# Performance work log

Measured on AMD Instinct MI355X. Metric: run time of the kernel, lower is better.

Reference implementation:

```python
import jax, jax.numpy as jnp
import numpy as np

B, N, F_IN, D = 32, 100, 10, 64
TAU = 10.0
ALPHA = 0.2  # GAT leaky-relu slope
EPS = 1e-8


def _cosine_sim(e):
    n = e / (jnp.linalg.norm(e, axis=-1, keepdims=True) + EPS)
    return n @ n.T


def _gumbel_softmax_hard(key, logits, tau):
    u = jax.random.uniform(key, logits.shape, minval=1e-20, maxval=1.0)
    g = -jnp.log(-jnp.log(u))
    y = jax.nn.softmax((logits + g) / tau, axis=-1)
    y_hard = jax.nn.one_hot(jnp.argmax(y, axis=-1), logits.shape[-1], dtype=y.dtype)
    # straight-through
    return y_hard + y - jax.lax.stop_gradient(y)


def _gat(x, adj, emb, W, b, a):
    # single GAT layer; attention keys are embedding-augmented features
    h = x @ W + b                       # (Nt, D)
    k = h + emb                         # (Nt, D)
    d = h.shape[-1]
    e = jax.nn.leaky_relu((k @ a[:d])[:, None] + (k @ a[d:])[None, :], ALPHA)  # (Nt, Nt)
    e = jnp.where(adj > 0, e, jnp.asarray(-9e15, e.dtype))
    att = jax.nn.softmax(e, axis=-1)
    hp = att @ h
    return jax.nn.elu(hp), att


def setup_inputs():
    key = jax.random.key(0)
    ks = jax.random.split(key, 12)
    s = 0.1
    return {
        "data": jax.random.normal(ks[0], (B, N, F_IN), jnp.float32),
        "node_emb": jax.random.normal(ks[1], (N, D), jnp.float32),
        "lin_W": jax.random.normal(ks[2], (F_IN, D), jnp.float32) * s,
        "lin_b": jnp.zeros((D,), jnp.float32),
        "gat_s_W": jax.random.normal(ks[3], (F_IN, D), jnp.float32) * s,
        "gat_s_b": jnp.zeros((D,), jnp.float32),
        "gat_s_a": jax.random.normal(ks[4], (2 * D,), jnp.float32) * s,
        "gat_d_W": jax.random.normal(ks[5], (F_IN, D), jnp.float32) * s,
        "gat_d_b": jnp.zeros((D,), jnp.float32),
        "gat_d_a": jax.random.normal(ks[6], (2 * D,), jnp.float32) * s,
        "bn_gamma": jnp.ones((D,), jnp.float32),
        "bn_beta": jnp.zeros((D,), jnp.float32),
        "out_W": jax.random.normal(ks[7], (D, 1), jnp.float32) * s,
        "out_b": jnp.zeros((1,), jnp.float32),
    }


def reference(data, node_emb, lin_W, lin_b, gat_s_W, gat_s_b, gat_s_a,
              gat_d_W, gat_d_b, gat_d_a, bn_gamma, bn_beta, out_W, out_b):
    k1, k2 = jax.random.split(jax.random.key(42))
    Nt = B * N
    x = data.reshape(Nt, F_IN)
    # block-diagonal mask: edges only within each batch sample
    blk = jnp.arange(Nt) // N
    mask = (blk[:, None] == blk[None, :]).astype(x.dtype)

    # --- static graph from node embeddings ---
    sim_s = _cosine_sim(node_emb)                       # (N, N)
    adj_s = _gumbel_softmax_hard(k1, jnp.stack([sim_s, 1.0 - sim_s], -1), TAU)[..., 0]
    adj_s = ((adj_s + jnp.eye(N, dtype=adj_s.dtype)) > 0).astype(x.dtype)  # bool->float (kills grad, as torch)
    adj_s = jnp.tile(adj_s, (B, B)) * mask              # (Nt, Nt)

    # --- dynamic graph from current features ---
    emb_d = x @ lin_W + lin_b                           # (Nt, D)
    sim_d = _cosine_sim(emb_d)                          # (Nt, Nt)
    adj_d = _gumbel_softmax_hard(k2, jnp.stack([sim_d, 1.0 - sim_d], -1), TAU)[..., 0]
    adj_d = adj_d * mask

    emb_rep = jnp.tile(node_emb, (B, 1))                # (Nt, D)
    emb_S, _ = _gat(x, adj_s, emb_rep, gat_s_W, gat_s_b, gat_s_a)
    emb_D, _ = _gat(x, adj_d, emb_rep, gat_d_W, gat_d_b, gat_d_a)
    emb = emb_S + 0.01 * emb_D                          # (Nt, D)

    out = emb.reshape(B, N, D) * node_emb               # (B, N, D)
    # BatchNorm1d over channel D (training-mode batch stats), then ReLU
    m = out.mean(axis=(0, 1))
    v = out.var(axis=(0, 1))
    out = (out - m) / jnp.sqrt(v + 1e-5) * bn_gamma + bn_beta
    out = jax.nn.relu(out)
    # dropout p=0.2 is identity in eval mode
    out = out @ out_W + out_b                           # (B, N, 1)
    return out.reshape(-1, N)                           # (B, N)
```

## Files before the change

kernel.cpp:

```cpp
#include <hip/hip_runtime.h>
#include <cstdint>

#define NT 3200
#define NN 100
#define FD 10
#define DD 64

__host__ __device__ inline void tf2x32(uint32_t ks0, uint32_t ks1, uint32_t x0,
                                       uint32_t x1, uint32_t& o0, uint32_t& o1) {
  uint32_t ks2 = ks0 ^ ks1 ^ 0x1BD11BDAu;
  x0 += ks0; x1 += ks1;
#define TF_RND(r) { x0 += x1; x1 = (x1 << (r)) | (x1 >> (32 - (r))); x1 ^= x0; }
  TF_RND(13) TF_RND(15) TF_RND(26) TF_RND(6)
  x0 += ks1; x1 += ks2 + 1u;
  TF_RND(17) TF_RND(29) TF_RND(16) TF_RND(24)
  x0 += ks2; x1 += ks0 + 2u;
  TF_RND(13) TF_RND(15) TF_RND(26) TF_RND(6)
  x0 += ks0; x1 += ks1 + 3u;
  TF_RND(17) TF_RND(29) TF_RND(16) TF_RND(24)
  x0 += ks1; x1 += ks2 + 4u;
  TF_RND(13) TF_RND(15) TF_RND(26) TF_RND(6)
  x0 += ks2; x1 += ks0 + 5u;
#undef TF_RND
  o0 = x0; o1 = x1;
}

__device__ inline float gumbel_noise(uint32_t ka, uint32_t kb, uint32_t cnt) {
  uint32_t o0, o1;
  tf2x32(ka, kb, 0u, cnt, o0, o1);
  uint32_t bits = o0 ^ o1;
  float u = __uint_as_float((bits >> 9) | 0x3F800000u) - 1.0f;
  u = fmaxf(u, 1e-20f);
  return -logf(-logf(u));
}

__global__ __launch_bounds__(256) void k_prep_adj(
    const float* __restrict__ x, const float* __restrict__ ne,
    const float* __restrict__ lW, const float* __restrict__ lb,
    const float* __restrict__ Ws, const float* __restrict__ bs,
    const float* __restrict__ as_, const float* __restrict__ Wd,
    const float* __restrict__ bd, const float* __restrict__ ad,
    float* __restrict__ h_s, float* __restrict__ h_d, float* __restrict__ nd,
    float* __restrict__ q_s, float* __restrict__ kk_s, float* __restrict__ q_d,
    float* __restrict__ kk_d, float* __restrict__ adjS, uint32_t k1a,
    uint32_t k1b) {
  __shared__ float sne[NN * 65];
  __shared__ float dnorm[NN];
  int tid = threadIdx.x, wid = tid >> 6, lane = tid & 63;
  int blk = blockIdx.x;
  if (blk < 800) {
    int i = blk * 4 + wid;
    const float* xr = x + i * FD;
    float hs = bs[lane], hd = bd[lane], ed = lb[lane];
#pragma unroll
    for (int f = 0; f < FD; ++f) {
      float xv = xr[f];
      hs = fmaf(xv, Ws[f * DD + lane], hs);
      hd = fmaf(xv, Wd[f * DD + lane], hd);
      ed = fmaf(xv, lW[f * DD + lane], ed);
    }
    h_s[i * DD + lane] = hs;
    h_d[i * DD + lane] = hd;
    float ss = ed * ed;
    for (int off = 32; off > 0; off >>= 1) ss += __shfl_xor(ss, off, 64);
    nd[i * DD + lane] = ed / (sqrtf(ss) + 1e-8f);
    int r = i % NN;
    float em = ne[r * DD + lane];
    float ks = hs + em, kd = hd + em;
    float qs = ks * as_[lane], kks = ks * as_[DD + lane];
    float qd = kd * ad[lane], kkd = kd * ad[DD + lane];
    for (int off = 32; off > 0; off >>= 1) {
      qs += __shfl_xor(qs, off, 64);
      kks += __shfl_xor(kks, off, 64);
      qd += __shfl_xor(qd, off, 64);
      kkd += __shfl_xor(kkd, off, 64);
    }
    if (lane == 0) { q_s[i] = qs; kk_s[i] = kks; q_d[i] = qd; kk_d[i] = kkd; }
  } else {
    for (int idx = tid; idx < NN * DD; idx += 256)
      sne[(idx >> 6) * 65 + (idx & 63)] = ne[idx];
    __syncthreads();
    for (int row = wid; row < NN; row += 4) {
      float v = sne[row * 65 + lane];
      float ss = v * v;
      for (int off = 32; off > 0; off >>= 1) ss += __shfl_xor(ss, off, 64);
      if (lane == 0) dnorm[row] = sqrtf(ss) + 1e-8f;
    }
    __syncthreads();
    for (int idx = tid; idx < NN * DD; idx += 256) {
      int row = idx >> 6;
      sne[row * 65 + (idx & 63)] /= dnorm[row];
    }
    __syncthreads();
    int p = (blk - 800) * 256 + tid;
    if (p < NN * NN) {
      int r = p / NN, c = p - r * NN;
      float sim = 0.0f;
#pragma unroll
      for (int k = 0; k < DD; ++k)
        sim = fmaf(sne[r * 65 + k], sne[c * 65 + k], sim);
      float g0 = gumbel_noise(k1a, k1b, (uint32_t)(2 * p));
      float g1 = gumbel_noise(k1a, k1b, (uint32_t)(2 * p + 1));
      bool edge = (sim + g0 >= 1.0f - sim + g1) || (r == c);
      adjS[p] = edge ? 1.0f : 0.0f;
    }
  }
}

__global__ __launch_bounds__(256) void k_attn(
    const float* __restrict__ h_s, const float* __restrict__ h_d,
    const float* __restrict__ nd, const float* __restrict__ q_s,
    const float* __restrict__ kk_s, const float* __restrict__ q_d,
    const float* __restrict__ kk_d, const float* __restrict__ adjS,
    const float* __restrict__ ne, float* __restrict__ o,
    float* __restrict__ gstat, uint32_t k2a, uint32_t k2b) {
  __shared__ float lnd[NN * 65];
  __shared__ float att[4][2][NN];
  int tid = threadIdx.x, wid = tid >> 6, lane = tid & 63;
  int blk = blockIdx.x;
  int b = blk / 25, rb = (blk % 25) * 4;
  int base = b * NN;
  for (int idx = tid; idx < NN * DD; idx += 256)
    lnd[(idx >> 6) * 65 + (idx & 63)] = nd[base * DD + idx];
  __syncthreads();

  int r = rb + wid;
  int i = base + r;
  float sqs = q_s[i], sqd = q_d[i];
  int j0 = lane, j1 = lane + 64;
  bool v1 = (j1 < NN);
  int jj1 = v1 ? j1 : 0;
  float sim0 = 0.0f, sim1 = 0.0f;
  const float* ndr = &lnd[r * 65];
  const float* nj0 = &lnd[j0 * 65];
  const float* nj1 = &lnd[jj1 * 65];
#pragma unroll
  for (int k = 0; k < DD; ++k) {
    float a = ndr[k];
    sim0 = fmaf(a, nj0[k], sim0);
    sim1 = fmaf(a, nj1[k], sim1);
  }
  float es0 = -9e15f, es1 = -9e15f, ed0 = -9e15f, ed1 = -9e15f;
  if (adjS[r * NN + j0] > 0.0f) {
    float v = sqs + kk_s[base + j0];
    es0 = (v >= 0.0f) ? v : 0.2f * v;
  }
  if (v1 && adjS[r * NN + j1] > 0.0f) {
    float v = sqs + kk_s[base + j1];
    es1 = (v >= 0.0f) ? v : 0.2f * v;
  }
  {
    uint32_t c0 = ((uint32_t)i * 3200u + (uint32_t)(base + j0)) * 2u;
    float g0 = gumbel_noise(k2a, k2b, c0);
    float g1 = gumbel_noise(k2a, k2b, c0 + 1u);
    if (sim0 + g0 >= 1.0f - sim0 + g1) {
      float v = sqd + kk_d[base + j0];
      ed0 = (v >= 0.0f) ? v : 0.2f * v;
    }
  }
  if (v1) {
    uint32_t c1 = ((uint32_t)i * 3200u + (uint32_t)(base + j1)) * 2u;
    float g0 = gumbel_noise(k2a, k2b, c1);
    float g1 = gumbel_noise(k2a, k2b, c1 + 1u);
    if (sim1 + g0 >= 1.0f - sim1 + g1) {
      float v = sqd + kk_d[base + j1];
      ed1 = (v >= 0.0f) ? v : 0.2f * v;
    }
  }
  float ms = fmaxf(es0, es1);
  for (int off = 32; off > 0; off >>= 1) ms = fmaxf(ms, __shfl_xor(ms, off, 64));
  float ws0 = expf(es0 - ms);
  float ws1 = v1 ? expf(es1 - ms) : 0.0f;
  float Ss = ws0 + ws1;
  for (int off = 32; off > 0; off >>= 1) Ss += __shfl_xor(Ss, off, 64);
  att[wid][0][j0] = ws0 / Ss;
  if (v1) att[wid][0][j1] = ws1 / Ss;
  float md = fmaxf(ed0, ed1);
  for (int off = 32; off > 0; off >>= 1) md = fmaxf(md, __shfl_xor(md, off, 64));
  float wd0 = expf(ed0 - md);
  float wd1 = v1 ? expf(ed1 - md) : 0.0f;
  float Sd = wd0 + wd1;
  for (int off = 32; off > 0; off >>= 1) Sd += __shfl_xor(Sd, off, 64);
  att[wid][1][j0] = wd0 / Sd;
  if (v1) att[wid][1][j1] = wd1 / Sd;
  float hs = 0.0f, hd2 = 0.0f;
  const float* hsp = h_s + base * DD + lane;
  const float* hdp = h_d + base * DD + lane;
#pragma unroll 4
  for (int j = 0; j < NN; ++j) {
    hs = fmaf(att[wid][0][j], hsp[j * DD], hs);
    hd2 = fmaf(att[wid][1][j], hdp[j * DD], hd2);
  }
  float eS = (hs > 0.0f) ? hs : expm1f(hs);
  float eD = (hd2 > 0.0f) ? hd2 : expm1f(hd2);
  float ov = (eS + 0.01f * eD) * ne[r * DD + lane];
  o[i * DD + lane] = ov;
  att[wid][0][lane] = ov;
  att[wid][1][lane] = ov * ov;
  __syncthreads();
  if (wid == 0) {
    float s = att[0][0][lane] + att[1][0][lane] + att[2][0][lane] + att[3][0][lane];
    unsafeAtomicAdd(&gstat[lane], s);
  } else if (wid == 1) {
    float s = att[0][1][lane] + att[1][1][lane] + att[2][1][lane] + att[3][1][lane];
    unsafeAtomicAdd(&gstat[64 + lane], s);
  }
}

__global__ __launch_bounds__(256) void k_final(
    const float* __restrict__ o, const float* __restrict__ gstat,
    const float* __restrict__ gamma, const float* __restrict__ beta,
    const float* __restrict__ outW, const float* __restrict__ outb,
    float* __restrict__ out) {
  int tid = threadIdx.x, wid = tid >> 6, lane = tid & 63;
  int i = blockIdx.x * 4 + wid;
  float m = gstat[lane] * (1.0f / NT);
  float ex2 = gstat[64 + lane] * (1.0f / NT);
  float var = ex2 - m * m;
  float scale = gamma[lane] / sqrtf(var + 1e-5f);
  float xv = o[i * DD + lane];
  float v = (xv - m) * scale + beta[lane];
  v = fmaxf(v, 0.0f);
  float p = v * outW[lane];
  for (int off = 32; off > 0; off >>= 1) p += __shfl_xor(p, off, 64);
  if (lane == 0) out[i] = p + outb[0];
}

extern "C" void kernel_launch(void* const* d_in, const int* in_sizes, int n_in,
                              void* d_out, int out_size, void* d_ws,
                              size_t ws_size, hipStream_t stream) {
  const float* data = (const float*)d_in[0];
  const float* node_emb = (const float*)d_in[1];
  const float* lin_W = (const float*)d_in[2];
  const float* lin_b = (const float*)d_in[3];
  const float* gat_s_W = (const float*)d_in[4];
  const float* gat_s_b = (const float*)d_in[5];
  const float* gat_s_a = (const float*)d_in[6];
  const float* gat_d_W = (const float*)d_in[7];
  const float* gat_d_b = (const float*)d_in[8];
  const float* gat_d_a = (const float*)d_in[9];
  const float* bn_gamma = (const float*)d_in[10];
  const float* bn_beta = (const float*)d_in[11];
  const float* out_W = (const float*)d_in[12];
  const float* out_b = (const float*)d_in[13];
  float* out = (float*)d_out;

  float* ws = (float*)d_ws;
  float* h_s = ws;
  float* h_d = ws + 204800;
  float* nd = ws + 409600;
  float* q_s = ws + 614400;
  float* kk_s = ws + 617600;
  float* q_d = ws + 620800;
  float* kk_d = ws + 624000;
  float* adjS = ws + 627200;
  float* o = ws + 637200;
  float* gstat = ws + 842000;

  uint32_t k1a, k1b, k2a, k2b;
  tf2x32(0u, 42u, 0u, 0u, k1a, k1b);
  tf2x32(0u, 42u, 0u, 1u, k2a, k2b);

  hipMemsetAsync(gstat, 0, 128 * sizeof(float), stream);
  k_prep_adj<<<840, 256, 0, stream>>>(data, node_emb, lin_W, lin_b, gat_s_W,
                                      gat_s_b, gat_s_a, gat_d_W, gat_d_b,
                                      gat_d_a, h_s, h_d, nd, q_s, kk_s, q_d,
                                      kk_d, adjS, k1a, k1b);
  k_attn<<<800, 256, 0, stream>>>(h_s, h_d, nd, q_s, kk_s, q_d, kk_d, adjS,
                                  node_emb, o, gstat, k2a, k2b);
  k_final<<<800, 256, 0, stream>>>(o, gstat, bn_gamma, bn_beta, out_W, out_b,
                                   out);
}
```

Baseline: 137.3 us.

## Fuse prep and attention kernels into one per-block recompute kernel

Merges the projection/adjacency prep kernel into the attention kernel. Each block now recomputes its batch's projections, normalized embeddings, the static-graph adjacency and the key scores in shared memory instead of reading them from global workspace. This removes one launch and the global round-trip for h_s, h_d, nd, q/kk and adjS. In exchange, every block redundantly recomputes the 100x100 static similarity and the per-batch projections, and shared memory use is higher, which may reduce occupancy.

```diff
diff --git a/kernel.cpp b/kernel.cpp
--- a/kernel.cpp
+++ b/kernel.cpp
@@ -34,138 +34,155 @@
   return -logf(-logf(u));
 }
 
-__global__ __launch_bounds__(256) void k_prep_adj(
+__global__ __launch_bounds__(256, 2) void k_main(
     const float* __restrict__ x, const float* __restrict__ ne,
     const float* __restrict__ lW, const float* __restrict__ lb,
     const float* __restrict__ Ws, const float* __restrict__ bs,
     const float* __restrict__ as_, const float* __restrict__ Wd,
     const float* __restrict__ bd, const float* __restrict__ ad,
-    float* __restrict__ h_s, float* __restrict__ h_d, float* __restrict__ nd,
-    float* __restrict__ q_s, float* __restrict__ kk_s, float* __restrict__ q_d,
-    float* __restrict__ kk_d, float* __restrict__ adjS, uint32_t k1a,
-    uint32_t k1b) {
-  __shared__ float sne[NN * 65];
-  __shared__ float dnorm[NN];
-  int tid = threadIdx.x, wid = tid >> 6, lane = tid & 63;
-  int blk = blockIdx.x;
-  if (blk < 800) {
-    int i = blk * 4 + wid;
-    const float* xr = x + i * FD;
-    float hs = bs[lane], hd = bd[lane], ed = lb[lane];
-#pragma unroll
-    for (int f = 0; f < FD; ++f) {
-      float xv = xr[f];
-      hs = fmaf(xv, Ws[f * DD + lane], hs);
-      hd = fmaf(xv, Wd[f * DD + lane], hd);
-      ed = fmaf(xv, lW[f * DD + lane], ed);
-    }
-    h_s[i * DD + lane] = hs;
-    h_d[i * DD + lane] = hd;
-    float ss = ed * ed;
-    for (int off = 32; off > 0; off >>= 1) ss += __shfl_xor(ss, off, 64);
-    nd[i * DD + lane] = ed / (sqrtf(ss) + 1e-8f);
-    int r = i % NN;
-    float em = ne[r * DD + lane];
-    float ks = hs + em, kd = hd + em;
-    float qs = ks * as_[lane], kks = ks * as_[DD + lane];
-    float qd = kd * ad[lane], kkd = kd * ad[DD + lane];
-    for (int off = 32; off > 0; off >>= 1) {
-      qs += __shfl_xor(qs, off, 64);
-      kks += __shfl_xor(kks, off, 64);
-      qd += __shfl_xor(qd, off, 64);
-      kkd += __shfl_xor(kkd, off, 64);
-    }
-    if (lane == 0) { q_s[i] = qs; kk_s[i] = kks; q_d[i] = qd; kk_d[i] = kkd; }
-  } else {
-    for (int idx = tid; idx < NN * DD; idx += 256)
-      sne[(idx >> 6) * 65 + (idx & 63)] = ne[idx];
-    __syncthreads();
-    for (int row = wid; row < NN; row += 4) {
-      float v = sne[row * 65 + lane];
-      float ss = v * v;
-      for (int off = 32; off > 0; off >>= 1) ss += __shfl_xor(ss, off, 64);
-      if (lane == 0) dnorm[row] = sqrtf(ss) + 1e-8f;
-    }
-    __syncthreads();
-    for (int idx = tid; idx < NN * DD; idx += 256) {
-      int row = idx >> 6;
-      sne[row * 65 + (idx & 63)] /= dnorm[row];
-    }
-    __syncthreads();
-    int p = (blk - 800) * 256 + tid;
-    if (p < NN * NN) {
-      int r = p / NN, c = p - r * NN;
-      float sim = 0.0f;
-#pragma unroll
-      for (int k = 0; k < DD; ++k)
-        sim = fmaf(sne[r * 65 + k], sne[c * 65 + k], sim);
-      float g0 = gumbel_noise(k1a, k1b, (uint32_t)(2 * p));
-      float g1 = gumbel_noise(k1a, k1b, (uint32_t)(2 * p + 1));
-      bool edge = (sim + g0 >= 1.0f - sim + g1) || (r == c);
-      adjS[p] = edge ? 1.0f : 0.0f;
-    }
-  }
-}
-
-__global__ __launch_bounds__(256) void k_attn(
-    const float* __restrict__ h_s, const float* __restrict__ h_d,
-    const float* __restrict__ nd, const float* __restrict__ q_s,
-    const float* __restrict__ kk_s, const float* __restrict__ q_d,
-    const float* __restrict__ kk_d, const float* __restrict__ adjS,
-    const float* __restrict__ ne, float* __restrict__ o,
-    float* __restrict__ gstat, uint32_t k2a, uint32_t k2b) {
-  __shared__ float lnd[NN * 65];
+    float* __restrict__ o, float* __restrict__ gstat, uint32_t k1a,
+    uint32_t k1b, uint32_t k2a, uint32_t k2b) {
+  __shared__ float sx[NN][FD];
+  __shared__ float A[NN * 65];
+  __shared__ float Bf[NN * 65];
+  __shared__ float kks[NN], kkd[NN], dnorm[NN];
   __shared__ float att[4][2][NN];
   int tid = threadIdx.x, wid = tid >> 6, lane = tid & 63;
   int blk = blockIdx.x;
   int b = blk / 25, rb = (blk % 25) * 4;
   int base = b * NN;
-  for (int idx = tid; idx < NN * DD; idx += 256)
-    lnd[(idx >> 6) * 65 + (idx & 63)] = nd[base * DD + idx];
-  __syncthreads();
-
   int r = rb + wid;
   int i = base + r;
-  float sqs = q_s[i], sqd = q_d[i];
   int j0 = lane, j1 = lane + 64;
   bool v1 = (j1 < NN);
   int jj1 = v1 ? j1 : 0;
-  float sim0 = 0.0f, sim1 = 0.0f;
-  const float* ndr = &lnd[r * 65];
-  const float* nj0 = &lnd[j0 * 65];
-  const float* nj1 = &lnd[jj1 * 65];
-#pragma unroll
-  for (int k = 0; k < DD; ++k) {
-    float a = ndr[k];
-    sim0 = fmaf(a, nj0[k], sim0);
-    sim1 = fmaf(a, nj1[k], sim1);
-  }
-  float es0 = -9e15f, es1 = -9e15f, ed0 = -9e15f, ed1 = -9e15f;
-  if (adjS[r * NN + j0] > 0.0f) {
-    float v = sqs + kk_s[base + j0];
-    es0 = (v >= 0.0f) ? v : 0.2f * v;
-  }
-  if (v1 && adjS[r * NN + j1] > 0.0f) {
-    float v = sqs + kk_s[base + j1];
-    es1 = (v >= 0.0f) ? v : 0.2f * v;
-  }
+
+  for (int idx = tid; idx < NN * FD; idx += 256)
+    ((float*)sx)[idx] = x[base * FD + idx];
+  for (int idx = tid; idx < NN * DD; idx += 256)
+    A[(idx >> 6) * 65 + (idx & 63)] = ne[idx];
+  __syncthreads();
+  for (int row = wid; row < NN; row += 4) {
+    float v = A[row * 65 + lane];
+    float ss = v * v;
+    for (int off = 32; off > 0; off >>= 1) ss += __shfl_xor(ss, off, 64);
+    if (lane == 0) dnorm[row] = sqrtf(ss) + 1e-8f;
+  }
+  __syncthreads();
+  for (int idx = tid; idx < NN * DD; idx += 256) {
+    int row = idx >> 6;
+    A[row * 65 + (idx & 63)] /= dnorm[row];
+  }
+  __syncthreads();
+
+  bool adj0, adj1;
   {
+    float s0 = 0.0f, s1 = 0.0f;
+#pragma unroll
+    for (int k = 0; k < DD; ++k) {
+      float a = A[r * 65 + k];
+      s0 = fmaf(a, A[j0 * 65 + k], s0);
+      s1 = fmaf(a, A[jj1 * 65 + k], s1);
+    }
+    int p0 = r * NN + j0;
+    float g0 = gumbel_noise(k1a, k1b, (uint32_t)(2 * p0));
+    float g1 = gumbel_noise(k1a, k1b, (uint32_t)(2 * p0 + 1));
+    adj0 = (s0 + g0 >= 1.0f - s0 + g1) || (r == j0);
+    int p1 = r * NN + jj1;
+    float g2 = gumbel_noise(k1a, k1b, (uint32_t)(2 * p1));
+    float g3 = gumbel_noise(k1a, k1b, (uint32_t)(2 * p1 + 1));
+    adj1 = v1 && ((s1 + g2 >= 1.0f - s1 + g3) || (r == j1));
+  }
+
+  float wWs[FD], wWd[FD], wlW[FD];
+#pragma unroll
+  for (int f = 0; f < FD; ++f) {
+    wWs[f] = Ws[f * DD + lane];
+    wWd[f] = Wd[f * DD + lane];
+    wlW[f] = lW[f * DD + lane];
+  }
+  float vbs = bs[lane], vbd = bd[lane], vlb = lb[lane];
+  float a0 = as_[lane], a1 = as_[DD + lane];
+  float d0 = ad[lane], d1 = ad[DD + lane];
+  float q_s_own = 0.0f, q_d_own = 0.0f;
+  __syncthreads();
+  for (int row = wid; row < NN; row += 4) {
+    float hs = vbs, hd = vbd, ed = vlb;
+#pragma unroll
+    for (int f = 0; f < FD; ++f) {
+      float xv = sx[row][f];
+      hs = fmaf(xv, wWs[f], hs);
+      hd = fmaf(xv, wWd[f], hd);
+      ed = fmaf(xv, wlW[f], ed);
+    }
+    float ss = ed * ed;
+    for (int off = 32; off > 0; off >>= 1) ss += __shfl_xor(ss, off, 64);
+    Bf[row * 65 + lane] = ed / (sqrtf(ss) + 1e-8f);
+    A[row * 65 + lane] = hs;
+    float em = ne[row * DD + lane];
+    float ks = hs + em, kd = hd + em;
+    float kksv = ks * a1, kkdv = kd * d1;
+    for (int off = 32; off > 0; off >>= 1) {
+      kksv += __shfl_xor(kksv, off, 64);
+      kkdv += __shfl_xor(kkdv, off, 64);
+    }
+    if (row == r) {
+      float qsv = ks * a0, qdv = kd * d0;
+      for (int off = 32; off > 0; off >>= 1) {
+        qsv += __shfl_xor(qsv, off, 64);
+        qdv += __shfl_xor(qdv, off, 64);
+      }
+      q_s_own = qsv;
+      q_d_own = qdv;
+    }
+    if (lane == 0) { kks[row] = kksv; kkd[row] = kkdv; }
+  }
+  __syncthreads();
+
+  bool dadj0, dadj1;
+  {
+    float s0 = 0.0f, s1 = 0.0f;
+#pragma unroll
+    for (int k = 0; k < DD; ++k) {
+      float a = Bf[r * 65 + k];
+      s0 = fmaf(a, Bf[j0 * 65 + k], s0);
+      s1 = fmaf(a, Bf[jj1 * 65 + k], s1);
+    }
     uint32_t c0 = ((uint32_t)i * 3200u + (uint32_t)(base + j0)) * 2u;
     float g0 = gumbel_noise(k2a, k2b, c0);
     float g1 = gumbel_noise(k2a, k2b, c0 + 1u);
-    if (sim0 + g0 >= 1.0f - sim0 + g1) {
-      float v = sqd + kk_d[base + j0];
-      ed0 = (v >= 0.0f) ? v : 0.2f * v;
-    }
-  }
-  if (v1) {
-    uint32_t c1 = ((uint32_t)i * 3200u + (uint32_t)(base + j1)) * 2u;
-    float g0 = gumbel_noise(k2a, k2b, c1);
-    float g1 = gumbel_noise(k2a, k2b, c1 + 1u);
-    if (sim1 + g0 >= 1.0f - sim1 + g1) {
-      float v = sqd + kk_d[base + j1];
-      ed1 = (v >= 0.0f) ? v : 0.2f * v;
-    }
+    dadj0 = (s0 + g0 >= 1.0f - s0 + g1);
+    uint32_t c1 = ((uint32_t)i * 3200u + (uint32_t)(base + jj1)) * 2u;
+    float g2 = gumbel_noise(k2a, k2b, c1);
+    float g3 = gumbel_noise(k2a, k2b, c1 + 1u);
+    dadj1 = v1 && (s1 + g2 >= 1.0f - s1 + g3);
+  }
+  __syncthreads();
+
+  for (int row = wid; row < NN; row += 4) {
+    float hd = vbd;
+#pragma unroll
+    for (int f = 0; f < FD; ++f) hd = fmaf(sx[row][f], wWd[f], hd);
+    Bf[row * 65 + lane] = hd;
+  }
+  __syncthreads();
+
+  float es0 = -9e15f, es1 = -9e15f, ed0 = -9e15f, ed1 = -9e15f;
+  if (adj0) {
+    float v = q_s_own + kks[j0];
+    es0 = (v >= 0.0f) ? v : 0.2f * v;
+  }
+  if (adj1) {
+    float v = q_s_own + kks[j1];
+    es1 = (v >= 0.0f) ? v : 0.2f * v;
+  }
+  if (dadj0) {
+    float v = q_d_own + kkd[j0];
+    ed0 = (v >= 0.0f) ? v : 0.2f * v;
+  }
+  if (dadj1) {
+    float v = q_d_own + kkd[j1];
+    ed1 = (v >= 0.0f) ? v : 0.2f * v;
   }
   float ms = fmaxf(es0, es1);
   for (int off = 32; off > 0; off >>= 1) ms = fmaxf(ms, __shfl_xor(ms, off, 64));
@@ -184,17 +201,17 @@
   att[wid][1][j0] = wd0 / Sd;
   if (v1) att[wid][1][j1] = wd1 / Sd;
   float hs = 0.0f, hd2 = 0.0f;
-  const float* hsp = h_s + base * DD + lane;
-  const float* hdp = h_d + base * DD + lane;
 #pragma unroll 4
   for (int j = 0; j < NN; ++j) {
-    hs = fmaf(att[wid][0][j], hsp[j * DD], hs);
-    hd2 = fmaf(att[wid][1][j], hdp[j * DD], hd2);
+    hs = fmaf(att[wid][0][j], A[j * 65 + lane], hs);
+    hd2 = fmaf(att[wid][1][j], Bf[j * 65 + lane], hd2);
   }
   float eS = (hs > 0.0f) ? hs : expm1f(hs);
   float eD = (hd2 > 0.0f) ? hd2 : expm1f(hd2);
   float ov = (eS + 0.01f * eD) * ne[r * DD + lane];
   o[i * DD + lane] = ov;
+
+  __syncthreads();
   att[wid][0][lane] = ov;
   att[wid][1][lane] = ov * ov;
   __syncthreads();
@@ -246,28 +263,17 @@
   float* out = (float*)d_out;
 
   float* ws = (float*)d_ws;
-  float* h_s = ws;
-  float* h_d = ws + 204800;
-  float* nd = ws + 409600;
-  float* q_s = ws + 614400;
-  float* kk_s = ws + 617600;
-  float* q_d = ws + 620800;
-  float* kk_d = ws + 624000;
-  float* adjS = ws + 627200;
-  float* o = ws + 637200;
-  float* gstat = ws + 842000;
+  float* o = ws;
+  float* gstat = ws + 204800;
 
   uint32_t k1a, k1b, k2a, k2b;
   tf2x32(0u, 42u, 0u, 0u, k1a, k1b);
   tf2x32(0u, 42u, 0u, 1u, k2a, k2b);
 
   hipMemsetAsync(gstat, 0, 128 * sizeof(float), stream);
-  k_prep_adj<<<840, 256, 0, stream>>>(data, node_emb, lin_W, lin_b, gat_s_W,
-                                      gat_s_b, gat_s_a, gat_d_W, gat_d_b,
-                                      gat_d_a, h_s, h_d, nd, q_s, kk_s, q_d,
-                                      kk_d, adjS, k1a, k1b);
-  k_attn<<<800, 256, 0, stream>>>(h_s, h_d, nd, q_s, kk_s, q_d, kk_d, adjS,
-                                  node_emb, o, gstat, k2a, k2b);
+  k_main<<<800, 256, 0, stream>>>(data, node_emb, lin_W, lin_b, gat_s_W,
+                                  gat_s_b, gat_s_a, gat_d_W, gat_d_b, gat_d_a,
+                                  o, gstat, k1a, k1b, k2a, k2b);
   k_final<<<800, 256, 0, stream>>>(o, gstat, bn_gamma, bn_beta, out_W, out_b,
                                    out);
 }
```

Result: slower. 172.2 us (+25.4%).

## Stage h_s/h_d in LDS with 10-row blocks and fold gstat zeroing into prep

Applied to the files above, without the earlier changes.

The attention kernel now handles 10 rows per block using 640 threads, so each batch needs 10 blocks instead of 25. After computing the similarities it reuses LDS to stage h_s and h_d, and it broadcasts attention weights with register shuffles instead of writing them to shared memory. The gstat memset is removed and done inside the prep kernel instead. This should cut redundant global reads of h and one launch, at the cost of larger blocks, an extra barrier and fewer blocks in flight.

```diff
diff --git a/kernel.cpp b/kernel.cpp
--- a/kernel.cpp
+++ b/kernel.cpp
@@ -42,8 +42,8 @@
     const float* __restrict__ bd, const float* __restrict__ ad,
     float* __restrict__ h_s, float* __restrict__ h_d, float* __restrict__ nd,
     float* __restrict__ q_s, float* __restrict__ kk_s, float* __restrict__ q_d,
-    float* __restrict__ kk_d, float* __restrict__ adjS, uint32_t k1a,
-    uint32_t k1b) {
+    float* __restrict__ kk_d, float* __restrict__ adjS,
+    float* __restrict__ gstat, uint32_t k1a, uint32_t k1b) {
   __shared__ float sne[NN * 65];
   __shared__ float dnorm[NN];
   int tid = threadIdx.x, wid = tid >> 6, lane = tid & 63;
@@ -77,6 +77,7 @@
     }
     if (lane == 0) { q_s[i] = qs; kk_s[i] = kks; q_d[i] = qd; kk_d[i] = kkd; }
   } else {
+    if (blk == 800 && tid < 128) gstat[tid] = 0.0f;
     for (int idx = tid; idx < NN * DD; idx += 256)
       sne[(idx >> 6) * 65 + (idx & 63)] = ne[idx];
     __syncthreads();
@@ -107,21 +108,22 @@
   }
 }
 
-__global__ __launch_bounds__(256) void k_attn(
+__global__ __launch_bounds__(640, 5) void k_attn(
     const float* __restrict__ h_s, const float* __restrict__ h_d,
     const float* __restrict__ nd, const float* __restrict__ q_s,
     const float* __restrict__ kk_s, const float* __restrict__ q_d,
     const float* __restrict__ kk_d, const float* __restrict__ adjS,
     const float* __restrict__ ne, float* __restrict__ o,
     float* __restrict__ gstat, uint32_t k2a, uint32_t k2b) {
-  __shared__ float lnd[NN * 65];
-  __shared__ float att[4][2][NN];
+  __shared__ float lA[NN * 65];
+  __shared__ float lB[NN * 65];
+  __shared__ float sums[2 * 10 * 64];
   int tid = threadIdx.x, wid = tid >> 6, lane = tid & 63;
   int blk = blockIdx.x;
-  int b = blk / 25, rb = (blk % 25) * 4;
+  int b = blk / 10, rb = (blk % 10) * 10;
   int base = b * NN;
-  for (int idx = tid; idx < NN * DD; idx += 256)
-    lnd[(idx >> 6) * 65 + (idx & 63)] = nd[base * DD + idx];
+  for (int idx = tid; idx < NN * DD; idx += 640)
+    lA[(idx >> 6) * 65 + (idx & 63)] = nd[base * DD + idx];
   __syncthreads();
 
   int r = rb + wid;
@@ -131,9 +133,9 @@
   bool v1 = (j1 < NN);
   int jj1 = v1 ? j1 : 0;
   float sim0 = 0.0f, sim1 = 0.0f;
-  const float* ndr = &lnd[r * 65];
-  const float* nj0 = &lnd[j0 * 65];
-  const float* nj1 = &lnd[jj1 * 65];
+  const float* ndr = &lA[r * 65];
+  const float* nj0 = &lA[j0 * 65];
+  const float* nj1 = &lA[jj1 * 65];
 #pragma unroll
   for (int k = 0; k < DD; ++k) {
     float a = ndr[k];
@@ -173,36 +175,49 @@
   float ws1 = v1 ? expf(es1 - ms) : 0.0f;
   float Ss = ws0 + ws1;
   for (int off = 32; off > 0; off >>= 1) Ss += __shfl_xor(Ss, off, 64);
-  att[wid][0][j0] = ws0 / Ss;
-  if (v1) att[wid][0][j1] = ws1 / Ss;
+  float a0s = ws0 / Ss, a1s = ws1 / Ss;
   float md = fmaxf(ed0, ed1);
   for (int off = 32; off > 0; off >>= 1) md = fmaxf(md, __shfl_xor(md, off, 64));
   float wd0 = expf(ed0 - md);
   float wd1 = v1 ? expf(ed1 - md) : 0.0f;
   float Sd = wd0 + wd1;
   for (int off = 32; off > 0; off >>= 1) Sd += __shfl_xor(Sd, off, 64);
-  att[wid][1][j0] = wd0 / Sd;
-  if (v1) att[wid][1][j1] = wd1 / Sd;
+  float a0d = wd0 / Sd, a1d = wd1 / Sd;
+
+  __syncthreads();
+  for (int idx = tid; idx < NN * DD; idx += 640) {
+    int row = idx >> 6, ch = idx & 63;
+    lA[row * 65 + ch] = h_s[base * DD + idx];
+    lB[row * 65 + ch] = h_d[base * DD + idx];
+  }
+  __syncthreads();
   float hs = 0.0f, hd2 = 0.0f;
-  const float* hsp = h_s + base * DD + lane;
-  const float* hdp = h_d + base * DD + lane;
 #pragma unroll 4
-  for (int j = 0; j < NN; ++j) {
-    hs = fmaf(att[wid][0][j], hsp[j * DD], hs);
-    hd2 = fmaf(att[wid][1][j], hdp[j * DD], hd2);
+  for (int j = 0; j < 64; ++j) {
+    hs = fmaf(__shfl(a0s, j, 64), lA[j * 65 + lane], hs);
+    hd2 = fmaf(__shfl(a0d, j, 64), lB[j * 65 + lane], hd2);
+  }
+#pragma unroll 4
+  for (int j = 0; j < 36; ++j) {
+    hs = fmaf(__shfl(a1s, j, 64), lA[(j + 64) * 65 + lane], hs);
+    hd2 = fmaf(__shfl(a1d, j, 64), lB[(j + 64) * 65 + lane], hd2);
   }
   float eS = (hs > 0.0f) ? hs : expm1f(hs);
   float eD = (hd2 > 0.0f) ? hd2 : expm1f(hd2);
   float ov = (eS + 0.01f * eD) * ne[r * DD + lane];
   o[i * DD + lane] = ov;
-  att[wid][0][lane] = ov;
-  att[wid][1][lane] = ov * ov;
+  sums[wid * 64 + lane] = ov;
+  sums[640 + wid * 64 + lane] = ov * ov;
   __syncthreads();
   if (wid == 0) {
-    float s = att[0][0][lane] + att[1][0][lane] + att[2][0][lane] + att[3][0][lane];
+    float s = 0.0f;
+#pragma unroll
+    for (int w = 0; w < 10; ++w) s += sums[w * 64 + lane];
     unsafeAtomicAdd(&gstat[lane], s);
   } else if (wid == 1) {
-    float s = att[0][1][lane] + att[1][1][lane] + att[2][1][lane] + att[3][1][lane];
+    float s = 0.0f;
+#pragma unroll
+    for (int w = 0; w < 10; ++w) s += sums[640 + w * 64 + lane];
     unsafeAtomicAdd(&gstat[64 + lane], s);
   }
 }
@@ -261,12 +276,11 @@
   tf2x32(0u, 42u, 0u, 0u, k1a, k1b);
   tf2x32(0u, 42u, 0u, 1u, k2a, k2b);
 
-  hipMemsetAsync(gstat, 0, 128 * sizeof(float), stream);
   k_prep_adj<<<840, 256, 0, stream>>>(data, node_emb, lin_W, lin_b, gat_s_W,
                                       gat_s_b, gat_s_a, gat_d_W, gat_d_b,
                                       gat_d_a, h_s, h_d, nd, q_s, kk_s, q_d,
-                                      kk_d, adjS, k1a, k1b);
-  k_attn<<<800, 256, 0, stream>>>(h_s, h_d, nd, q_s, kk_s, q_d, kk_d, adjS,
+                                      kk_d, adjS, gstat, k1a, k1b);
+  k_attn<<<320, 640, 0, stream>>>(h_s, h_d, nd, q_s, kk_s, q_d, kk_d, adjS,
                                   node_emb, o, gstat, k2a, k2b);
   k_final<<<800, 256, 0, stream>>>(o, gstat, bn_gamma, bn_beta, out_W, out_b,
                                    out);
```

Measured after the change: 189.6 us. 38.1% more time.

## Move similarity, gumbel sampling and masked logits into per-batch prep kernel

Applied to the files above, without the earlier changes.

The prep kernel is restructured so that each block handles a quarter of one batch sample. It computes the projected features, normalized embeddings, both the static and dynamic adjacency samples, and the masked leaky-relu logits, which it writes as full NxN matrices. The attention kernel then only loads the precomputed logits for the softmax and aggregation. The gstat zeroing replaces the separate memset launch. In exchange, the static similarity and noise work is recomputed per batch, the grid shrinks to 128 blocks, and extra global traffic is added for the logit matrices.

```diff
diff --git a/kernel.cpp b/kernel.cpp
--- a/kernel.cpp
+++ b/kernel.cpp
@@ -34,38 +34,59 @@
   return -logf(-logf(u));
 }
 
-__global__ __launch_bounds__(256) void k_prep_adj(
+__global__ __launch_bounds__(512) void k_prep(
     const float* __restrict__ x, const float* __restrict__ ne,
     const float* __restrict__ lW, const float* __restrict__ lb,
     const float* __restrict__ Ws, const float* __restrict__ bs,
     const float* __restrict__ as_, const float* __restrict__ Wd,
     const float* __restrict__ bd, const float* __restrict__ ad,
-    float* __restrict__ h_s, float* __restrict__ h_d, float* __restrict__ nd,
-    float* __restrict__ q_s, float* __restrict__ kk_s, float* __restrict__ q_d,
-    float* __restrict__ kk_d, float* __restrict__ adjS, uint32_t k1a,
-    uint32_t k1b) {
-  __shared__ float sne[NN * 65];
-  __shared__ float dnorm[NN];
+    float* __restrict__ h_s, float* __restrict__ h_d, float* __restrict__ esM,
+    float* __restrict__ edM, float* __restrict__ gstat, uint32_t k1a,
+    uint32_t k1b, uint32_t k2a, uint32_t k2b) {
+  __shared__ float sx[NN][FD];
+  __shared__ float nen[NN * 65];
+  __shared__ float snd[NN * 65];
+  __shared__ float skk_s[NN], skk_d[NN], sq_s[NN], sq_d[NN], dnorm[NN];
   int tid = threadIdx.x, wid = tid >> 6, lane = tid & 63;
   int blk = blockIdx.x;
-  if (blk < 800) {
-    int i = blk * 4 + wid;
-    const float* xr = x + i * FD;
+  int b = blk >> 2, q = blk & 3;
+  int base = b * NN;
+  if (blk == 0 && tid < 128) gstat[tid] = 0.0f;
+
+  for (int idx = tid; idx < NN * FD; idx += 512)
+    ((float*)sx)[idx] = x[base * FD + idx];
+  for (int idx = tid; idx < NN * DD; idx += 512)
+    nen[(idx >> 6) * 65 + (idx & 63)] = ne[idx];
+  __syncthreads();
+  for (int row = wid; row < NN; row += 8) {
+    float v = nen[row * 65 + lane];
+    float ss = v * v;
+    for (int off = 32; off > 0; off >>= 1) ss += __shfl_xor(ss, off, 64);
+    if (lane == 0) dnorm[row] = sqrtf(ss) + 1e-8f;
+  }
+  __syncthreads();
+  for (int idx = tid; idx < NN * DD; idx += 512) {
+    int row = idx >> 6;
+    nen[row * 65 + (idx & 63)] /= dnorm[row];
+  }
+  for (int row = wid; row < NN; row += 8) {
     float hs = bs[lane], hd = bd[lane], ed = lb[lane];
 #pragma unroll
     for (int f = 0; f < FD; ++f) {
-      float xv = xr[f];
+      float xv = sx[row][f];
       hs = fmaf(xv, Ws[f * DD + lane], hs);
       hd = fmaf(xv, Wd[f * DD + lane], hd);
       ed = fmaf(xv, lW[f * DD + lane], ed);
     }
-    h_s[i * DD + lane] = hs;
-    h_d[i * DD + lane] = hd;
+    int gi = base + row;
+    if (row / 25 == q) {
+      h_s[gi * DD + lane] = hs;
+      h_d[gi * DD + lane] = hd;
+    }
     float ss = ed * ed;
     for (int off = 32; off > 0; off >>= 1) ss += __shfl_xor(ss, off, 64);
-    nd[i * DD + lane] = ed / (sqrtf(ss) + 1e-8f);
-    int r = i % NN;
-    float em = ne[r * DD + lane];
+    snd[row * 65 + lane] = ed / (sqrtf(ss) + 1e-8f);
+    float em = ne[row * DD + lane];
     float ks = hs + em, kd = hd + em;
     float qs = ks * as_[lane], kks = ks * as_[DD + lane];
     float qd = kd * ad[lane], kkd = kd * ad[DD + lane];
@@ -75,98 +96,62 @@
       qd += __shfl_xor(qd, off, 64);
       kkd += __shfl_xor(kkd, off, 64);
     }
-    if (lane == 0) { q_s[i] = qs; kk_s[i] = kks; q_d[i] = qd; kk_d[i] = kkd; }
-  } else {
-    for (int idx = tid; idx < NN * DD; idx += 256)
-      sne[(idx >> 6) * 65 + (idx & 63)] = ne[idx];
-    __syncthreads();
-    for (int row = wid; row < NN; row += 4) {
-      float v = sne[row * 65 + lane];
-      float ss = v * v;
-      for (int off = 32; off > 0; off >>= 1) ss += __shfl_xor(ss, off, 64);
-      if (lane == 0) dnorm[row] = sqrtf(ss) + 1e-8f;
-    }
-    __syncthreads();
-    for (int idx = tid; idx < NN * DD; idx += 256) {
-      int row = idx >> 6;
-      sne[row * 65 + (idx & 63)] /= dnorm[row];
-    }
-    __syncthreads();
-    int p = (blk - 800) * 256 + tid;
-    if (p < NN * NN) {
-      int r = p / NN, c = p - r * NN;
-      float sim = 0.0f;
+    if (lane == 0) {
+      sq_s[row] = qs; skk_s[row] = kks; sq_d[row] = qd; skk_d[row] = kkd;
+    }
+  }
+  __syncthreads();
+  for (int p = tid; p < 25 * NN; p += 512) {
+    int lr = p / NN, c = p - lr * NN;
+    int r = q * 25 + lr;
+    int i = base + r;
+    float sim = 0.0f;
 #pragma unroll
-      for (int k = 0; k < DD; ++k)
-        sim = fmaf(sne[r * 65 + k], sne[c * 65 + k], sim);
-      float g0 = gumbel_noise(k1a, k1b, (uint32_t)(2 * p));
-      float g1 = gumbel_noise(k1a, k1b, (uint32_t)(2 * p + 1));
-      bool edge = (sim + g0 >= 1.0f - sim + g1) || (r == c);
-      adjS[p] = edge ? 1.0f : 0.0f;
-    }
+    for (int k = 0; k < DD; ++k)
+      sim = fmaf(nen[r * 65 + k], nen[c * 65 + k], sim);
+    uint32_t ps = (uint32_t)(r * NN + c);
+    float g0 = gumbel_noise(k1a, k1b, 2u * ps);
+    float g1 = gumbel_noise(k1a, k1b, 2u * ps + 1u);
+    bool edge = (sim + g0 >= 1.0f - sim + g1) || (r == c);
+    float es = -9e15f;
+    if (edge) {
+      float v = sq_s[r] + skk_s[c];
+      es = (v >= 0.0f) ? v : 0.2f * v;
+    }
+    esM[i * NN + c] = es;
+    float sd = 0.0f;
+#pragma unroll
+    for (int k = 0; k < DD; ++k)
+      sd = fmaf(snd[r * 65 + k], snd[c * 65 + k], sd);
+    uint32_t cd = ((uint32_t)i * 3200u + (uint32_t)(base + c)) * 2u;
+    float h0 = gumbel_noise(k2a, k2b, cd);
+    float h1 = gumbel_noise(k2a, k2b, cd + 1u);
+    float edv = -9e15f;
+    if (sd + h0 >= 1.0f - sd + h1) {
+      float v = sq_d[r] + skk_d[c];
+      edv = (v >= 0.0f) ? v : 0.2f * v;
+    }
+    edM[i * NN + c] = edv;
   }
 }
 
 __global__ __launch_bounds__(256) void k_attn(
     const float* __restrict__ h_s, const float* __restrict__ h_d,
-    const float* __restrict__ nd, const float* __restrict__ q_s,
-    const float* __restrict__ kk_s, const float* __restrict__ q_d,
-    const float* __restrict__ kk_d, const float* __restrict__ adjS,
+    const float* __restrict__ esM, const float* __restrict__ edM,
     const float* __restrict__ ne, float* __restrict__ o,
-    float* __restrict__ gstat, uint32_t k2a, uint32_t k2b) {
-  __shared__ float lnd[NN * 65];
+    float* __restrict__ gstat) {
   __shared__ float att[4][2][NN];
   int tid = threadIdx.x, wid = tid >> 6, lane = tid & 63;
   int blk = blockIdx.x;
-  int b = blk / 25, rb = (blk % 25) * 4;
+  int i = blk * 4 + wid;
+  int b = i / NN, r = i - b * NN;
   int base = b * NN;
-  for (int idx = tid; idx < NN * DD; idx += 256)
-    lnd[(idx >> 6) * 65 + (idx & 63)] = nd[base * DD + idx];
-  __syncthreads();
-
-  int r = rb + wid;
-  int i = base + r;
-  float sqs = q_s[i], sqd = q_d[i];
   int j0 = lane, j1 = lane + 64;
   bool v1 = (j1 < NN);
-  int jj1 = v1 ? j1 : 0;
-  float sim0 = 0.0f, sim1 = 0.0f;
-  const float* ndr = &lnd[r * 65];
-  const float* nj0 = &lnd[j0 * 65];
-  const float* nj1 = &lnd[jj1 * 65];
-#pragma unroll
-  for (int k = 0; k < DD; ++k) {
-    float a = ndr[k];
-    sim0 = fmaf(a, nj0[k], sim0);
-    sim1 = fmaf(a, nj1[k], sim1);
-  }
-  float es0 = -9e15f, es1 = -9e15f, ed0 = -9e15f, ed1 = -9e15f;
-  if (adjS[r * NN + j0] > 0.0f) {
-    float v = sqs + kk_s[base + j0];
-    es0 = (v >= 0.0f) ? v : 0.2f * v;
-  }
-  if (v1 && adjS[r * NN + j1] > 0.0f) {
-    float v = sqs + kk_s[base + j1];
-    es1 = (v >= 0.0f) ? v : 0.2f * v;
-  }
-  {
-    uint32_t c0 = ((uint32_t)i * 3200u + (uint32_t)(base + j0)) * 2u;
-    float g0 = gumbel_noise(k2a, k2b, c0);
-    float g1 = gumbel_noise(k2a, k2b, c0 + 1u);
-    if (sim0 + g0 >= 1.0f - sim0 + g1) {
-      float v = sqd + kk_d[base + j0];
-      ed0 = (v >= 0.0f) ? v : 0.2f * v;
-    }
-  }
-  if (v1) {
-    uint32_t c1 = ((uint32_t)i * 3200u + (uint32_t)(base + j1)) * 2u;
-    float g0 = gumbel_noise(k2a, k2b, c1);
-    float g1 = gumbel_noise(k2a, k2b, c1 + 1u);
-    if (sim1 + g0 >= 1.0f - sim1 + g1) {
-      float v = sqd + kk_d[base + j1];
-      ed1 = (v >= 0.0f) ? v : 0.2f * v;
-    }
-  }
+  float es0 = esM[i * NN + j0];
+  float es1 = v1 ? esM[i * NN + j1] : -9e15f;
+  float ed0 = edM[i * NN + j0];
+  float ed1 = v1 ? edM[i * NN + j1] : -9e15f;
   float ms = fmaxf(es0, es1);
   for (int off = 32; off > 0; off >>= 1) ms = fmaxf(ms, __shfl_xor(ms, off, 64));
   float ws0 = expf(es0 - ms);
@@ -195,6 +180,7 @@
   float eD = (hd2 > 0.0f) ? hd2 : expm1f(hd2);
   float ov = (eS + 0.01f * eD) * ne[r * DD + lane];
   o[i * DD + lane] = ov;
+  __syncthreads();
   att[wid][0][lane] = ov;
   att[wid][1][lane] = ov * ov;
   __syncthreads();
@@ -248,26 +234,20 @@
   float* ws = (float*)d_ws;
   float* h_s = ws;
   float* h_d = ws + 204800;
-  float* nd = ws + 409600;
-  float* q_s = ws + 614400;
-  float* kk_s = ws + 617600;
-  float* q_d = ws + 620800;
-  float* kk_d = ws + 624000;
-  float* adjS = ws + 627200;
-  float* o = ws + 637200;
-  float* gstat = ws + 842000;
+  float* esM = ws + 409600;
+  float* edM = ws + 729600;
+  float* o = ws + 1049600;
+  float* gstat = ws + 1254400;
 
   uint32_t k1a, k1b, k2a, k2b;
   tf2x32(0u, 42u, 0u, 0u, k1a, k1b);
   tf2x32(0u, 42u, 0u, 1u, k2a, k2b);
 
-  hipMemsetAsync(gstat, 0, 128 * sizeof(float), stream);
-  k_prep_adj<<<840, 256, 0, stream>>>(data, node_emb, lin_W, lin_b, gat_s_W,
-                                      gat_s_b, gat_s_a, gat_d_W, gat_d_b,
-                                      gat_d_a, h_s, h_d, nd, q_s, kk_s, q_d,
-                                      kk_d, adjS, k1a, k1b);
-  k_attn<<<800, 256, 0, stream>>>(h_s, h_d, nd, q_s, kk_s, q_d, kk_d, adjS,
-                                  node_emb, o, gstat, k2a, k2b);
+  k_prep<<<128, 512, 0, stream>>>(data, node_emb, lin_W, lin_b, gat_s_W,
+                                  gat_s_b, gat_s_a, gat_d_W, gat_d_b, gat_d_a,
+                                  h_s, h_d, esM, edM, gstat, k1a, k1b, k2a,
+                                  k2b);
+  k_attn<<<800, 256, 0, stream>>>(h_s, h_d, esM, edM, node_emb, o, gstat);
   k_final<<<800, 256, 0, stream>>>(o, gstat, bn_gamma, bn_beta, out_W, out_b,
                                    out);
 }
```

Result: slower. 146.2 us (+6.5%).
